# Performance work log

Measured on AMD Instinct MI355X. Metric: run time of the kernel, lower is better.

## Reference

```python
import jax, jax.numpy as jnp
import numpy as np

NUM_HEADS = 32
NUM_KV_HEADS = 8
HEAD_DIM = 128
HIDDEN = 4096
ROPE_THETA = 10000.0
SLIDING_WINDOW = 1024
NEG_INF = -1e9


def _make_sliding_window_mask(q_len, kv_len, window):
    # additive mask: 0 where attendable (causal AND within window), -inf otherwise
    i = jnp.arange(q_len)[:, None]
    j = jnp.arange(kv_len)[None, :]
    allowed = (j <= i) & (j > i - window)
    return jnp.where(allowed, 0.0, NEG_INF).astype(jnp.float32)[None, None]  # [1,1,q,kv]


def _rope_tables(seq_len, head_dim, theta):
    inv_freq = 1.0 / (theta ** (jnp.arange(0, head_dim, 2, dtype=jnp.float32) / head_dim))
    t = jnp.arange(seq_len, dtype=jnp.float32)
    freqs = jnp.einsum('i,j->ij', t, inv_freq)        # [S, D/2]
    emb = jnp.concatenate([freqs, freqs], axis=-1)     # [S, D]
    return jnp.cos(emb), jnp.sin(emb)


def _rotate_half(x):
    d = x.shape[-1] // 2
    return jnp.concatenate([-x[..., d:], x[..., :d]], axis=-1)


def setup_inputs() -> dict:
    key = jax.random.key(0)
    ks = jax.random.split(key, 5)
    B, S = 1, 2048
    sc = 0.02
    hidden_states = jax.random.normal(ks[0], (B, S, HIDDEN), dtype=jnp.float32)
    Wq = jax.random.normal(ks[1], (HIDDEN, NUM_HEADS * HEAD_DIM), dtype=jnp.float32) * sc
    Wk = jax.random.normal(ks[2], (HIDDEN, NUM_KV_HEADS * HEAD_DIM), dtype=jnp.float32) * sc
    Wv = jax.random.normal(ks[3], (HIDDEN, NUM_KV_HEADS * HEAD_DIM), dtype=jnp.float32) * sc
    Wo = jax.random.normal(ks[4], (NUM_HEADS * HEAD_DIM, HIDDEN), dtype=jnp.float32) * sc
    attention_mask = _make_sliding_window_mask(S, S, SLIDING_WINDOW)
    position_ids = jnp.arange(S, dtype=jnp.int64)[None, :]
    return {"hidden_states": hidden_states, "attention_mask": attention_mask,
            "position_ids": position_ids, "Wq": Wq, "Wk": Wk, "Wv": Wv, "Wo": Wo}


def reference(hidden_states, attention_mask, position_ids, Wq, Wk, Wv, Wo):
    B, S, _ = hidden_states.shape
    # projections
    q = (hidden_states @ Wq).reshape(B, S, NUM_HEADS, HEAD_DIM).transpose(0, 2, 1, 3)      # [B,H,S,D]
    k = (hidden_states @ Wk).reshape(B, S, NUM_KV_HEADS, HEAD_DIM).transpose(0, 2, 1, 3)   # [B,Hk,S,D]
    v = (hidden_states @ Wv).reshape(B, S, NUM_KV_HEADS, HEAD_DIM).transpose(0, 2, 1, 3)
    # RoPE
    cos_t, sin_t = _rope_tables(S, HEAD_DIM, ROPE_THETA)
    cos = cos_t[position_ids][:, None]  # [B,1,S,D]
    sin = sin_t[position_ids][:, None]
    q = q * cos + _rotate_half(q) * sin
    k = k * cos + _rotate_half(k) * sin
    # repeat_kv (GQA): [B,Hk,S,D] -> [B,H,S,D]
    n_rep = NUM_HEADS // NUM_KV_HEADS
    k = jnp.repeat(k, n_rep, axis=1)
    v = jnp.repeat(v, n_rep, axis=1)
    # attention
    scores = jnp.einsum('bhqd,bhkd->bhqk', q, k) / np.sqrt(HEAD_DIM)
    scores = scores + attention_mask
    probs = jax.nn.softmax(scores, axis=-1)
    out = jnp.einsum('bhqk,bhkd->bhqd', probs, v)
    out = out.transpose(0, 2, 1, 3).reshape(B, S, HIDDEN)
    return out @ Wo
```

## Files before the change

kernel.cpp:

```cpp
#include <hip/hip_runtime.h>

typedef __attribute__((ext_vector_type(8))) short short8;
typedef __attribute__((ext_vector_type(4))) short s16x4;
typedef __attribute__((ext_vector_type(4))) float f32x4;
typedef unsigned short u16;
typedef unsigned int u32;

__device__ __forceinline__ u16 f2bf(float f) {
  union { float f; unsigned int u; } v; v.f = f;
  unsigned int r = (v.u + 0x7FFFu + ((v.u >> 16) & 1u)) >> 16;
  return (u16)r;
}
__device__ __forceinline__ float bf2f(u16 b) {
  union { unsigned int u; float f; } v; v.u = ((unsigned int)b) << 16;
  return v.f;
}
__device__ __forceinline__ void load_lds16(const void* g, void* l) {
  __builtin_amdgcn_global_load_lds((const __attribute__((address_space(1))) void*)g,
                                   (__attribute__((address_space(3))) void*)l, 16, 0, 0);
}

__global__ void cvt_f32_bf16_kernel(const float* __restrict__ in, u16* __restrict__ out, int n4) {
  int i = blockIdx.x * blockDim.x + threadIdx.x;
  if (i >= n4) return;
  float4 v = ((const float4*)in)[i];
  ushort4 o;
  o.x = f2bf(v.x); o.y = f2bf(v.y); o.z = f2bf(v.z); o.w = f2bf(v.w);
  ((ushort4*)out)[i] = o;
}

__device__ __forceinline__ void tconv64_tile(const float* __restrict__ W, u16* __restrict__ Wt,
                                             int K, int N, int nb, int kb, int tid) {
  __shared__ float tile[64][65];
  int tx = tid & 15, ty = tid >> 4;
  const float* src = W + (size_t)(kb + ty) * N + nb + tx * 4;
#pragma unroll
  for (int i = 0; i < 4; ++i) {
    float4 v = *(const float4*)(src + (size_t)i * 16 * N);
    tile[ty + i * 16][tx * 4 + 0] = v.x;
    tile[ty + i * 16][tx * 4 + 1] = v.y;
    tile[ty + i * 16][tx * 4 + 2] = v.z;
    tile[ty + i * 16][tx * 4 + 3] = v.w;
  }
  __syncthreads();
  u16* dst = Wt + (size_t)(nb + ty) * K + kb + tx * 4;
#pragma unroll
  for (int i = 0; i < 4; ++i) {
    s16x4 o;
#pragma unroll
    for (int j = 0; j < 4; ++j) o[j] = (short)f2bf(tile[tx * 4 + j][ty + i * 16]);
    *(s16x4*)(dst + (size_t)i * 16 * K) = o;
  }
}

__global__ void tconv3_kernel(const float* __restrict__ Wq, const float* __restrict__ Wk,
                              const float* __restrict__ Wv, u16* __restrict__ WqT,
                              u16* __restrict__ WkvT) {
  int id = blockIdx.x;
  if (id < 4096)      tconv64_tile(Wq, WqT, 4096, 4096, (id & 63) * 64, (id >> 6) * 64, threadIdx.x);
  else if (id < 5120) { int t = id - 4096; tconv64_tile(Wk, WkvT, 4096, 1024, (t & 15) * 64, (t >> 4) * 64, threadIdx.x); }
  else                { int t = id - 5120; tconv64_tile(Wv, WkvT + (size_t)1024 * 4096, 4096, 1024, (t & 15) * 64, (t >> 4) * 64, threadIdx.x); }
}

__global__ void tconv1_kernel(const float* __restrict__ W, u16* __restrict__ Wt) {
  int id = blockIdx.x;
  tconv64_tile(W, Wt, 4096, 4096, (id & 63) * 64, (id >> 6) * 64, threadIdx.x);
}

__global__ void rope_kernel(u16* __restrict__ Qb, u16* __restrict__ Kb) {
  int idx = blockIdx.x * blockDim.x + threadIdx.x;
  u16* X; int ld, hmask, hshift, id; float scale;
  if (idx < 4194304) { X = Qb; ld = 4096; hmask = 31; hshift = 5; id = idx;           scale = 0.12751781828987514f; }
  else               { X = Kb; ld = 1024; hmask = 7;  hshift = 3; id = idx - 4194304; scale = 1.0f; }
  int j = id & 63;
  int t = id >> 6;
  int hh = t & hmask;
  int s = t >> hshift;
  float invf = exp2f(-(float)j * (13.287712379549449f / 64.0f));
  float ang = (float)s * invf;
  float sn, cs;
  sincosf(ang, &sn, &cs);
  u16* p = X + (size_t)s * ld + hh * 128 + j;
  float a = bf2f(p[0]), b = bf2f(p[64]);
  p[0]  = f2bf((a * cs - b * sn) * scale);
  p[64] = f2bf((b * cs + a * sn) * scale);
}

__global__ __launch_bounds__(256, 2) void gemm_kv_kernel(
    const u16* __restrict__ A, const u16* __restrict__ B,
    u16* __restrict__ Kb, u16* __restrict__ Vt, int N, int K) {
  __shared__ u16 As[2][128 * 64];
  __shared__ u16 Bs[2][128 * 64];
  int tid = threadIdx.x, lane = tid & 63, w = tid >> 6;
  int wr = w >> 1, wc = w & 1;
  int g = lane >> 4, q = lane & 15;
  int nbx = gridDim.x;
  int flat = blockIdx.y * nbx + blockIdx.x;
  int cpx = (nbx * gridDim.y) >> 3;
  flat = (flat & 7) * cpx + (flat >> 3);
  int m0 = (flat / nbx) * 128, n0 = (flat % nbx) * 128;
  f32x4 acc[4][4];
#pragma unroll
  for (int i = 0; i < 4; ++i)
#pragma unroll
    for (int j = 0; j < 4; ++j) acc[i][j] = (f32x4){0.f, 0.f, 0.f, 0.f};
  int srow = tid >> 3;
  int scol = ((tid & 7) ^ (srow & 7)) << 3;
  const u16* ga = A + (size_t)(m0 + srow) * K + scol;
  const u16* gb = B + (size_t)(n0 + srow) * K + scol;
  int xorm = (q & 7) << 3;
  int arow = wr * 64 + q;
  int brow = wc * 64 + q;
  int nt = K >> 6;

  auto stage = [&](int buf, int t) {
    const u16* pa = ga + t * 64;
    const u16* pb = gb + t * 64;
#pragma unroll
    for (int it = 0; it < 4; ++it) {
      load_lds16(pa + (size_t)it * 32 * K, (char*)(&As[buf][0]) + (it * 256 + w * 64) * 16);
      load_lds16(pb + (size_t)it * 32 * K, (char*)(&Bs[buf][0]) + (it * 256 + w * 64) * 16);
    }
  };

  stage(0, 0);
  stage(1, 1);
  asm volatile("s_waitcnt vmcnt(8)" ::: "memory");
  __builtin_amdgcn_s_barrier();
  for (int t = 0; t < nt; ++t) {
    int cur = t & 1;
    short8 af[2][4], bfr[2][4];
#pragma unroll
    for (int kb = 0; kb < 2; ++kb) {
      int col = (kb * 32 + g * 8) ^ xorm;
#pragma unroll
      for (int m = 0; m < 4; ++m) af[kb][m]  = *(const short8*)&As[cur][(arow + m * 16) * 64 + col];
#pragma unroll
      for (int n = 0; n < 4; ++n) bfr[kb][n] = *(const short8*)&Bs[cur][(brow + n * 16) * 64 + col];
    }
    asm volatile("s_waitcnt lgkmcnt(0)" ::: "memory");
    __builtin_amdgcn_s_barrier();
    if (t + 2 < nt) stage(cur, t + 2);
    __builtin_amdgcn_sched_barrier(0);
    __builtin_amdgcn_s_setprio(1);
#pragma unroll
    for (int kb = 0; kb < 2; ++kb)
#pragma unroll
      for (int m = 0; m < 4; ++m)
#pragma unroll
        for (int n = 0; n < 4; ++n)
          acc[m][n] = __builtin_amdgcn_mfma_f32_16x16x32_bf16(af[kb][m], bfr[kb][n], acc[m][n], 0, 0, 0);
    __builtin_amdgcn_s_setprio(0);
    if (t + 2 < nt)      { asm volatile("s_waitcnt vmcnt(8)" ::: "memory"); }
    else if (t + 1 < nt) { asm volatile("s_waitcnt vmcnt(0)" ::: "memory"); }
    __builtin_amdgcn_s_barrier();
  }
  int crow = m0 + wr * 64 + g * 4;
  int ccol = n0 + wc * 64 + q;
  if (n0 < 1024) {
#pragma unroll
    for (int m = 0; m < 4; ++m)
#pragma unroll
      for (int n = 0; n < 4; ++n)
#pragma unroll
        for (int r = 0; r < 4; ++r)
          Kb[(size_t)(crow + m * 16 + r) * 1024 + ccol + n * 16] = f2bf(acc[m][n][r]);
  } else {
#pragma unroll
    for (int n = 0; n < 4; ++n) {
      int vcol = ccol + n * 16 - 1024;
#pragma unroll
      for (int m = 0; m < 4; ++m) {
        s16x4 o;
#pragma unroll
        for (int r = 0; r < 4; ++r) o[r] = (short)f2bf(acc[m][n][r]);
        *(s16x4*)(Vt + (size_t)vcol * 2048 + crow + m * 16) = o;
      }
    }
  }
}

template<int OUTF32>
__global__ __launch_bounds__(512, 2) void gemm_wide_kernel(
    const u16* __restrict__ A, const u16* __restrict__ B,
    void* __restrict__ C, int N, int K) {
  __shared__ u16 As[2][128 * 64];
  __shared__ u16 Bs[2][256 * 64];
  int tid = threadIdx.x, lane = tid & 63, wid = tid >> 6;
  int wr = wid >> 2, wc = wid & 3;
  int g = lane >> 4, q = lane & 15;
  int nbx = gridDim.x;
  int id = blockIdx.y * nbx + blockIdx.x;
  int cpx = (nbx * gridDim.y) >> 3;
  int swz = (id & 7) * cpx + (id >> 3);
  int m0 = (swz / nbx) * 128, n0 = (swz % nbx) * 256;
  f32x4 acc[4][4];
#pragma unroll
  for (int i = 0; i < 4; ++i)
#pragma unroll
    for (int j = 0; j < 4; ++j) acc[i][j] = (f32x4){0.f, 0.f, 0.f, 0.f};
  int srow = tid >> 3;
  int scol = ((tid & 7) ^ (srow & 7)) << 3;
  const u16* ga = A + (size_t)(m0 + srow) * K + scol;
  const u16* gb = B + (size_t)(n0 + srow) * K + scol;
  int xorm = (q & 7) << 3;
  int nt = K >> 6;

  auto stage = [&](int buf, int t) {
    const u16* pa = ga + t * 64;
    const u16* pb = gb + t * 64;
#pragma unroll
    for (int it = 0; it < 2; ++it)
      load_lds16(pa + (size_t)it * 64 * K, (char*)(&As[buf][0]) + it * 8192 + tid * 16);
#pragma unroll
    for (int it = 0; it < 4; ++it)
      load_lds16(pb + (size_t)it * 64 * K, (char*)(&Bs[buf][0]) + it * 8192 + tid * 16);
  };

  stage(0, 0);
  stage(1, 1);
  asm volatile("s_waitcnt vmcnt(6)" ::: "memory");
  __builtin_amdgcn_s_barrier();
  for (int t = 0; t < nt; ++t) {
    int cur = t & 1;
    short8 av[2][4], bv[2][4];
#pragma unroll
    for (int kb = 0; kb < 2; ++kb) {
      int col = (kb * 32 + g * 8) ^ xorm;
#pragma unroll
      for (int fm = 0; fm < 4; ++fm)
        av[kb][fm] = *(const short8*)&As[cur][(wr * 64 + fm * 16 + q) * 64 + col];
#pragma unroll
      for (int fn = 0; fn < 4; ++fn)
        bv[kb][fn] = *(const short8*)&Bs[cur][(wc * 64 + fn * 16 + q) * 64 + col];
    }
    asm volatile("s_waitcnt lgkmcnt(0)" ::: "memory");
    __builtin_amdgcn_s_barrier();
    if (t + 2 < nt) stage(cur, t + 2);
    __builtin_amdgcn_sched_barrier(0);
    __builtin_amdgcn_s_setprio(1);
#pragma unroll
    for (int kb = 0; kb < 2; ++kb)
#pragma unroll
      for (int fm = 0; fm < 4; ++fm)
#pragma unroll
        for (int fn = 0; fn < 4; ++fn)
          acc[fm][fn] = __builtin_amdgcn_mfma_f32_16x16x32_bf16(av[kb][fm], bv[kb][fn], acc[fm][fn], 0, 0, 0);
    __builtin_amdgcn_s_setprio(0);
    if (t + 2 < nt)      { asm volatile("s_waitcnt vmcnt(6)" ::: "memory"); }
    else if (t + 1 < nt) { asm volatile("s_waitcnt vmcnt(0)" ::: "memory"); }
    __builtin_amdgcn_s_barrier();
  }
  int crow = m0 + wr * 64 + g * 4;
  int ccol = n0 + wc * 64 + q;
#pragma unroll
  for (int fm = 0; fm < 4; ++fm)
#pragma unroll
    for (int fn = 0; fn < 4; ++fn)
#pragma unroll
      for (int r = 0; r < 4; ++r) {
        size_t off = (size_t)(crow + fm * 16 + r) * N + ccol + fn * 16;
        if (OUTF32) ((float*)C)[off] = acc[fm][fn][r];
        else        ((u16*)C)[off]   = f2bf(acc[fm][fn][r]);
      }
}

__global__ __launch_bounds__(256, 2) void attn_kernel(
    const u16* __restrict__ Q, const u16* __restrict__ Kg,
    const u16* __restrict__ Vt, u16* __restrict__ O) {
  __shared__ u16 Ks[2][64 * 128];
  __shared__ u16 Vs[2][128 * 64];
  int tid = threadIdx.x, lane = tid & 63, w = tid >> 6;
  int g = lane >> 4, q = lane & 15;
  int q0 = blockIdx.x * 64;
  int h = blockIdx.y, hk = h >> 2;
  int qrow = q0 + w * 16;
  int xorm = (lane & 7) << 3;
  short8 qf[4];
  {
    const u16* qp = Q + (size_t)(qrow + q) * 4096 + h * 128 + g * 8;
#pragma unroll
    for (int kk = 0; kk < 4; ++kk) qf[kk] = *(const short8*)(qp + kk * 32);
  }
  float mrow = -1e30f, lsum = 0.f;
  f32x4 of[8];
#pragma unroll
  for (int d = 0; d < 8; ++d) of[d] = (f32x4){0.f, 0.f, 0.f, 0.f};
  int jt_lo = (q0 >= 1024) ? ((q0 - 1023) >> 6) : 0;
  int jt_hi = q0 >> 6;
  int krow = tid >> 4;
  int kchunk = (tid & 15) ^ (krow & 7);
  const u16* kbase = Kg + (size_t)krow * 1024 + hk * 128 + (kchunk << 3);
  int vrow = tid >> 3;
  int vchunk = (tid & 7) ^ (vrow & 7);
  const u16* vbase = Vt + (size_t)(hk * 128 + vrow) * 2048 + (vchunk << 3);

  auto stageK = [&](int buf, int j0) {
    const u16* gp = kbase + (size_t)j0 * 1024;
#pragma unroll
    for (int it = 0; it < 4; ++it)
      load_lds16(gp + (size_t)it * 16 * 1024, (char*)(&Ks[buf][0]) + (it * 256 + w * 64) * 16);
  };
  auto stageV = [&](int buf, int j0) {
    const u16* gp = vbase + j0;
#pragma unroll
    for (int it = 0; it < 4; ++it)
      load_lds16(gp + (size_t)it * 32 * 2048, (char*)(&Vs[buf][0]) + (it * 256 + w * 64) * 16);
  };

  int cur = 0;
  stageK(0, jt_lo << 6);
  stageV(0, jt_lo << 6);
  asm volatile("s_waitcnt vmcnt(0)" ::: "memory");
  __syncthreads();
  for (int jt = jt_lo; jt <= jt_hi; ++jt) {
    int j0 = jt << 6;
    if (jt < jt_hi) { stageK(cur ^ 1, j0 + 64); stageV(cur ^ 1, j0 + 64); }
    f32x4 sf[4];
#pragma unroll
    for (int nt = 0; nt < 4; ++nt) sf[nt] = (f32x4){0.f, 0.f, 0.f, 0.f};
    const u16* ks = &Ks[cur][0];
    __builtin_amdgcn_s_setprio(1);
#pragma unroll
    for (int kk = 0; kk < 4; ++kk) {
      short8 qv = qf[kk];
      int col = (kk * 32 + g * 8) ^ xorm;
#pragma unroll
      for (int nt = 0; nt < 4; ++nt) {
        short8 kf = *(const short8*)&ks[(nt * 16 + q) * 128 + col];
        sf[nt] = __builtin_amdgcn_mfma_f32_16x16x32_bf16(kf, qv, sf[nt], 0, 0, 0);
      }
    }
    __builtin_amdgcn_s_setprio(0);
    float p[4][4];
#pragma unroll
    for (int nt = 0; nt < 4; ++nt)
#pragma unroll
      for (int r = 0; r < 4; ++r) p[nt][r] = sf[nt][r];
    if (j0 + 63 > qrow || j0 + 1009 <= qrow) {
      int qq = qrow + q;
      int kb = j0 + g * 4;
#pragma unroll
      for (int nt = 0; nt < 4; ++nt)
#pragma unroll
        for (int r = 0; r < 4; ++r) {
          int key = kb + nt * 16 + r;
          if (key > qq || key + 1024 <= qq) p[nt][r] = -1e9f;
        }
    }
    float tm = p[0][0];
#pragma unroll
    for (int nt = 0; nt < 4; ++nt)
#pragma unroll
      for (int r = 0; r < 4; ++r) tm = fmaxf(tm, p[nt][r]);
    tm = fmaxf(tm, __shfl_xor(tm, 16));
    tm = fmaxf(tm, __shfl_xor(tm, 32));
    if (__any(tm > mrow + 8.f)) {
      float nm = fmaxf(mrow, tm);
      float sc = __builtin_amdgcn_exp2f(mrow - nm);
      mrow = nm;
      lsum *= sc;
#pragma unroll
      for (int d = 0; d < 8; ++d) of[d] *= sc;
    }
    float ps = 0.f;
#pragma unroll
    for (int nt = 0; nt < 4; ++nt)
#pragma unroll
      for (int r = 0; r < 4; ++r) {
        float e = __builtin_amdgcn_exp2f(p[nt][r] - mrow);
        p[nt][r] = e;
        ps += e;
      }
    ps += __shfl_xor(ps, 16);
    ps += __shfl_xor(ps, 32);
    lsum += ps;
    u32 pk[4][2];
#pragma unroll
    for (int nt = 0; nt < 4; ++nt) {
      pk[nt][0] = __builtin_amdgcn_perm(__float_as_uint(p[nt][1]), __float_as_uint(p[nt][0]), 0x07060302u);
      pk[nt][1] = __builtin_amdgcn_perm(__float_as_uint(p[nt][3]), __float_as_uint(p[nt][2]), 0x07060302u);
    }
    int s0 = q + ((g & 1) ? 32 : 0);
    int s1 = s0 + 16;
    bool hi_sel = g >= 2;
    const u16* vs = &Vs[cur][0];
    __builtin_amdgcn_s_setprio(1);
#pragma unroll
    for (int kh = 0; kh < 2; ++kh) {
      int lo = kh * 2, hi = lo + 1;
      u32 a0 = (u32)__shfl((int)pk[lo][0], s0);
      u32 a1 = (u32)__shfl((int)pk[lo][1], s0);
      u32 b0 = (u32)__shfl((int)pk[hi][0], s0);
      u32 b1 = (u32)__shfl((int)pk[hi][1], s0);
      u32 a2 = (u32)__shfl((int)pk[lo][0], s1);
      u32 a3 = (u32)__shfl((int)pk[lo][1], s1);
      u32 b2 = (u32)__shfl((int)pk[hi][0], s1);
      u32 b3 = (u32)__shfl((int)pk[hi][1], s1);
      union { u32 u[4]; short8 s; } pb;
      pb.u[0] = hi_sel ? b0 : a0;
      pb.u[1] = hi_sel ? b1 : a1;
      pb.u[2] = hi_sel ? b2 : a2;
      pb.u[3] = hi_sel ? b3 : a3;
      int col = (kh * 32 + g * 8) ^ xorm;
#pragma unroll
      for (int dt = 0; dt < 8; ++dt) {
        short8 vv = *(const short8*)&vs[(dt * 16 + q) * 64 + col];
        of[dt] = __builtin_amdgcn_mfma_f32_16x16x32_bf16(vv, pb.s, of[dt], 0, 0, 0);
      }
    }
    __builtin_amdgcn_s_setprio(0);
    asm volatile("s_waitcnt vmcnt(0)" ::: "memory");
    __builtin_amdgcn_s_barrier();
    cur ^= 1;
  }
  float inv = 1.f / lsum;
  u16* op = O + (size_t)(qrow + q) * 4096 + h * 128 + g * 4;
#pragma unroll
  for (int dt = 0; dt < 8; ++dt) {
    s16x4 o4;
#pragma unroll
    for (int r = 0; r < 4; ++r) o4[r] = (short)f2bf(of[dt][r] * inv);
    *(s16x4*)(op + dt * 16) = o4;
  }
}

extern "C" void kernel_launch(void* const* d_in, const int* in_sizes, int n_in,
                              void* d_out, int out_size, void* d_ws, size_t ws_size,
                              hipStream_t stream) {
  (void)in_sizes; (void)n_in; (void)out_size;
  const float* hs = (const float*)d_in[0];
  const float* Wq = (const float*)d_in[3];
  const float* Wk = (const float*)d_in[4];
  const float* Wv = (const float*)d_in[5];
  const float* Wo = (const float*)d_in[6];
  float* out = (float*)d_out;
  char* ws = (char*)d_ws;

  u16* Xb   = (u16*)(ws + 0);
  u16* Wt   = (u16*)(ws + 16777216);
  u16* WkvT = (u16*)(ws + 50331648);
  u16* Qb   = (u16*)(ws + 67108864);
  u16* Kb   = (u16*)(ws + 83886080);
  u16* Vtb  = (u16*)(ws + 88080384);
  u16* Ab   = (u16*)(ws + 96468992);
  if (ws_size < 113246208u) return;

  cvt_f32_bf16_kernel<<<dim3(2097152 / 256), 256, 0, stream>>>(hs, Xb, 2097152);

  tconv3_kernel<<<dim3(6144), 256, 0, stream>>>(Wq, Wk, Wv, Wt, WkvT);

  gemm_wide_kernel<0><<<dim3(16, 16), 512, 0, stream>>>(Xb, Wt, Qb, 4096, 4096);

  gemm_kv_kernel<<<dim3(16, 16), 256, 0, stream>>>(Xb, WkvT, Kb, Vtb, 2048, 4096);

  rope_kernel<<<dim3(20480), 256, 0, stream>>>(Qb, Kb);

  attn_kernel<<<dim3(32, 32), 256, 0, stream>>>(Qb, Kb, Vtb, Ab);

  tconv1_kernel<<<dim3(4096), 256, 0, stream>>>(Wo, Wt);
  gemm_wide_kernel<1><<<dim3(16, 16), 512, 0, stream>>>(Ab, Wt, out, 4096, 4096);
}
```

Before: 340.6 us.

## Software-pipeline LDS fragment reads with MFMA in both GEMM kernels

Splits each 64-wide K tile into two 32-wide halves in both GEMM main loops, so the LDS reads for the second half overlap the MFMAs of the first half. The first half of the next tile is prefetched right after the barrier, keeping the matrix units fed while LDS loads are in flight. It also relaxes the wide GEMM's launch bound from 2 to 1 blocks per CU, giving the compiler more registers for the extra fragment buffers at the cost of occupancy.

```diff
diff --git a/kernel.cpp b/kernel.cpp
--- a/kernel.cpp
+++ b/kernel.cpp
@@ -122,38 +122,43 @@
       load_lds16(pb + (size_t)it * 32 * K, (char*)(&Bs[buf][0]) + (it * 256 + w * 64) * 16);
     }
   };
-
+  auto readF = [&](int cur, int kb, short8 (&af)[4], short8 (&bf)[4]) {
+    int col = (kb * 32 + g * 8) ^ xorm;
+#pragma unroll
+    for (int m = 0; m < 4; ++m) af[m] = *(const short8*)&As[cur][(arow + m * 16) * 64 + col];
+#pragma unroll
+    for (int n = 0; n < 4; ++n) bf[n] = *(const short8*)&Bs[cur][(brow + n * 16) * 64 + col];
+  };
+  auto domfma = [&](short8 (&af)[4], short8 (&bf)[4]) {
+    __builtin_amdgcn_s_setprio(1);
+#pragma unroll
+    for (int m = 0; m < 4; ++m)
+#pragma unroll
+      for (int n = 0; n < 4; ++n)
+        acc[m][n] = __builtin_amdgcn_mfma_f32_16x16x32_bf16(af[m], bf[n], acc[m][n], 0, 0, 0);
+    __builtin_amdgcn_s_setprio(0);
+  };
+
+  short8 afC[4], bfC[4], afN[4], bfN[4];
   stage(0, 0);
   stage(1, 1);
   asm volatile("s_waitcnt vmcnt(8)" ::: "memory");
   __builtin_amdgcn_s_barrier();
+  readF(0, 0, afC, bfC);
   for (int t = 0; t < nt; ++t) {
     int cur = t & 1;
-    short8 af[2][4], bfr[2][4];
-#pragma unroll
-    for (int kb = 0; kb < 2; ++kb) {
-      int col = (kb * 32 + g * 8) ^ xorm;
-#pragma unroll
-      for (int m = 0; m < 4; ++m) af[kb][m]  = *(const short8*)&As[cur][(arow + m * 16) * 64 + col];
-#pragma unroll
-      for (int n = 0; n < 4; ++n) bfr[kb][n] = *(const short8*)&Bs[cur][(brow + n * 16) * 64 + col];
-    }
+    readF(cur, 1, afN, bfN);
+    __builtin_amdgcn_sched_barrier(0);
+    domfma(afC, bfC);
     asm volatile("s_waitcnt lgkmcnt(0)" ::: "memory");
     __builtin_amdgcn_s_barrier();
     if (t + 2 < nt) stage(cur, t + 2);
     __builtin_amdgcn_sched_barrier(0);
-    __builtin_amdgcn_s_setprio(1);
-#pragma unroll
-    for (int kb = 0; kb < 2; ++kb)
-#pragma unroll
-      for (int m = 0; m < 4; ++m)
-#pragma unroll
-        for (int n = 0; n < 4; ++n)
-          acc[m][n] = __builtin_amdgcn_mfma_f32_16x16x32_bf16(af[kb][m], bfr[kb][n], acc[m][n], 0, 0, 0);
-    __builtin_amdgcn_s_setprio(0);
+    domfma(afN, bfN);
     if (t + 2 < nt)      { asm volatile("s_waitcnt vmcnt(8)" ::: "memory"); }
     else if (t + 1 < nt) { asm volatile("s_waitcnt vmcnt(0)" ::: "memory"); }
     __builtin_amdgcn_s_barrier();
+    if (t + 1 < nt) readF(cur ^ 1, 0, afC, bfC);
   }
   int crow = m0 + wr * 64 + g * 4;
   int ccol = n0 + wc * 64 + q;
@@ -181,7 +186,7 @@
 }
 
 template<int OUTF32>
-__global__ __launch_bounds__(512, 2) void gemm_wide_kernel(
+__global__ __launch_bounds__(512, 1) void gemm_wide_kernel(
     const u16* __restrict__ A, const u16* __restrict__ B,
     void* __restrict__ C, int N, int K) {
   __shared__ u16 As[2][128 * 64];
@@ -216,40 +221,45 @@
     for (int it = 0; it < 4; ++it)
       load_lds16(pb + (size_t)it * 64 * K, (char*)(&Bs[buf][0]) + it * 8192 + tid * 16);
   };
-
+  auto readF = [&](int cur, int kb, short8 (&av)[4], short8 (&bv)[4]) {
+    int col = (kb * 32 + g * 8) ^ xorm;
+#pragma unroll
+    for (int fm = 0; fm < 4; ++fm)
+      av[fm] = *(const short8*)&As[cur][(wr * 64 + fm * 16 + q) * 64 + col];
+#pragma unroll
+    for (int fn = 0; fn < 4; ++fn)
+      bv[fn] = *(const short8*)&Bs[cur][(wc * 64 + fn * 16 + q) * 64 + col];
+  };
+  auto domfma = [&](short8 (&av)[4], short8 (&bv)[4]) {
+    __builtin_amdgcn_s_setprio(1);
+#pragma unroll
+    for (int fm = 0; fm < 4; ++fm)
+#pragma unroll
+      for (int fn = 0; fn < 4; ++fn)
+        acc[fm][fn] = __builtin_amdgcn_mfma_f32_16x16x32_bf16(av[fm], bv[fn], acc[fm][fn], 0, 0, 0);
+    __builtin_amdgcn_s_setprio(0);
+  };
+
+  short8 avC[4], bvC[4], avN[4], bvN[4];
   stage(0, 0);
   stage(1, 1);
   asm volatile("s_waitcnt vmcnt(6)" ::: "memory");
   __builtin_amdgcn_s_barrier();
+  readF(0, 0, avC, bvC);
   for (int t = 0; t < nt; ++t) {
     int cur = t & 1;
-    short8 av[2][4], bv[2][4];
-#pragma unroll
-    for (int kb = 0; kb < 2; ++kb) {
-      int col = (kb * 32 + g * 8) ^ xorm;
-#pragma unroll
-      for (int fm = 0; fm < 4; ++fm)
-        av[kb][fm] = *(const short8*)&As[cur][(wr * 64 + fm * 16 + q) * 64 + col];
-#pragma unroll
-      for (int fn = 0; fn < 4; ++fn)
-        bv[kb][fn] = *(const short8*)&Bs[cur][(wc * 64 + fn * 16 + q) * 64 + col];
-    }
+    readF(cur, 1, avN, bvN);
+    __builtin_amdgcn_sched_barrier(0);
+    domfma(avC, bvC);
     asm volatile("s_waitcnt lgkmcnt(0)" ::: "memory");
     __builtin_amdgcn_s_barrier();
     if (t + 2 < nt) stage(cur, t + 2);
     __builtin_amdgcn_sched_barrier(0);
-    __builtin_amdgcn_s_setprio(1);
-#pragma unroll
-    for (int kb = 0; kb < 2; ++kb)
-#pragma unroll
-      for (int fm = 0; fm < 4; ++fm)
-#pragma unroll
-        for (int fn = 0; fn < 4; ++fn)
-          acc[fm][fn] = __builtin_amdgcn_mfma_f32_16x16x32_bf16(av[kb][fm], bv[kb][fn], acc[fm][fn], 0, 0, 0);
-    __builtin_amdgcn_s_setprio(0);
+    domfma(avN, bvN);
     if (t + 2 < nt)      { asm volatile("s_waitcnt vmcnt(6)" ::: "memory"); }
     else if (t + 1 < nt) { asm volatile("s_waitcnt vmcnt(0)" ::: "memory"); }
     __builtin_amdgcn_s_barrier();
+    if (t + 1 < nt) readF(cur ^ 1, 0, avC, bvC);
   }
   int crow = m0 + wr * 64 + g * 4;
   int ccol = n0 + wc * 64 + q;
```

After: 362.7 us. +6.5%, slower.
